# Kernel optimization log

Hardware: AMD Instinct MI355X
Metric: run time of the kernel (lower is better)

## Reference

```python
import jax, jax.numpy as jnp
import numpy as np

KERNEL_MUL = 2.0
KERNEL_NUM = 5


def _mmd(src, tar):
    """Multi-bandwidth Gaussian-kernel MMD, matching torch MMDLoss.mmd."""
    B = src.shape[0]
    total = jnp.concatenate([src, tar], axis=0)          # [2B, D]
    sq = jnp.sum(total * total, axis=1)                  # [2B]
    # ||a-b||^2 = ||a||^2 + ||b||^2 - 2 a.b  (GEMM form of the broadcast subtract)
    dist = sq[:, None] + sq[None, :] - 2.0 * (total @ total.T)  # [2B, 2B]
    n = 2 * B
    # torch uses L2_distance.data -> bandwidth is detached from the graph
    bandwidth = jax.lax.stop_gradient(jnp.sum(dist)) / (n * n - n)
    bandwidth = bandwidth / (KERNEL_MUL ** (KERNEL_NUM // 2))
    kernel = sum(jnp.exp(-dist / (bandwidth * KERNEL_MUL ** k)) for k in range(KERNEL_NUM))
    XX = kernel[:B, :B]
    YY = kernel[B:, B:]
    XY = kernel[:B, B:]
    YX = kernel[B:, :B]
    return jnp.mean(XX + YY - XY - YX)


def setup_inputs() -> dict:
    key = jax.random.key(0)
    k1, k2, k3 = jax.random.split(key, 3)
    B, IN, OUT, L = 4096, 512, 256, 2
    x = jax.random.normal(k1, (B, IN), dtype=jnp.float32)
    W_aux = jax.random.normal(k2, (L, IN), dtype=jnp.float32) * (1.0 / np.sqrt(IN))
    b_aux = jnp.zeros((L,), dtype=jnp.float32)
    W = jax.random.normal(k3, (L, OUT, IN), dtype=jnp.float32) * (1.0 / np.sqrt(IN))
    b = jnp.zeros((L, OUT), dtype=jnp.float32)
    return {"x": x, "W_aux": W_aux, "b_aux": b_aux, "W": W, "b": b}


def reference(x, W_aux, b_aux, W, b):
    L = W.shape[0]
    gates = jax.nn.softmax(x @ W_aux.T + b_aux, axis=-1)      # [B, L]
    outs = jnp.einsum('bi,loi->blo', x, W) + b                # [B, L, out]
    combine = jnp.einsum('bl,blo->bo', gates, outs)           # soft-gated combine
    loss = 0.0
    for i in range(L):
        for j in range(i + 1, L):
            loss = loss + _mmd(outs[:, i, :], outs[:, j, :])
    inter_mmd = loss * 2.0 / (L * L - L)
    return combine, -inter_mmd
```

## Files before the change

kernel.cpp:

```cpp
#include <hip/hip_runtime.h>
#include <stdint.h>
#include <math.h>

typedef __attribute__((ext_vector_type(8))) __bf16 bf16x8;
typedef __attribute__((ext_vector_type(4))) __bf16 bf16x4;
typedef __attribute__((ext_vector_type(4))) float f32x4;

__device__ __forceinline__ void gload_lds16(const __bf16* g, __bf16* l) {
  __builtin_amdgcn_global_load_lds(
      (const __attribute__((address_space(1))) unsigned int*)g,
      (__attribute__((address_space(3))) unsigned int*)l,
      16, 0, 0);
}

__global__ __launch_bounds__(256) void k_gates(const float* __restrict__ x,
                                               const float* __restrict__ Waux,
                                               const float* __restrict__ baux,
                                               float* __restrict__ gates) {
  const int wave = threadIdx.x >> 6;
  const int lane = threadIdx.x & 63;
  const int row = blockIdx.x * 4 + wave;
  const float4* xr = (const float4*)(x + (size_t)row * 512);
  const float4* w0 = (const float4*)(Waux);
  const float4* w1 = (const float4*)(Waux + 512);
  float p0 = 0.f, p1 = 0.f;
  for (int c = lane; c < 128; c += 64) {
    float4 xv = xr[c];
    float4 a = w0[c], b = w1[c];
    p0 += xv.x * a.x + xv.y * a.y + xv.z * a.z + xv.w * a.w;
    p1 += xv.x * b.x + xv.y * b.y + xv.z * b.z + xv.w * b.w;
  }
  for (int off = 32; off; off >>= 1) {
    p0 += __shfl_down(p0, off, 64);
    p1 += __shfl_down(p1, off, 64);
  }
  if (lane == 0) {
    p0 += baux[0]; p1 += baux[1];
    float m = fmaxf(p0, p1);
    float e0 = __expf(p0 - m), e1 = __expf(p1 - m);
    float inv = 1.f / (e0 + e1);
    gates[row * 2 + 0] = e0 * inv;
    gates[row * 2 + 1] = e1 * inv;
  }
}

__global__ __launch_bounds__(256) void k_outs(const float* __restrict__ x,
                                              const float* __restrict__ W,
                                              const float* __restrict__ bias,
                                              __bf16* __restrict__ totalbf) {
  __shared__ __bf16 As[64][64];
  __shared__ __bf16 Bs[64][64];
  const int bj = blockIdx.x;
  const int bi = blockIdx.y;
  const int t = threadIdx.x;
  const int wid = t >> 6, lane = t & 63;
  const int wr = wid >> 1, wc = wid & 1;
  const int n16 = lane & 15, q = lane >> 4;
  const int sx = (n16 & 7) << 3;
  const int erow = t >> 4;
  const int c4 = (t & 15) << 2;

  f32x4 acc[2][2];
  f32x4 zero = {0.f, 0.f, 0.f, 0.f};
  for (int i = 0; i < 2; ++i)
    for (int j = 0; j < 2; ++j) acc[i][j] = zero;

  const int arow0 = bi * 64, brow0 = bj * 64;

  float4 ra[4], rb[4];
#pragma unroll
  for (int p = 0; p < 4; ++p) {
    int row = p * 16 + erow;
    ra[p] = *(const float4*)(x + (size_t)(arow0 + row) * 512 + c4);
    rb[p] = *(const float4*)(W + (size_t)(brow0 + row) * 512 + c4);
  }

  for (int kc = 0; kc < 512; kc += 64) {
#pragma unroll
    for (int p = 0; p < 4; ++p) {
      int row = p * 16 + erow;
      int col = c4 ^ ((row & 7) << 3);
      float4 va = ra[p];
      bf16x4 ba = {(__bf16)va.x, (__bf16)va.y, (__bf16)va.z, (__bf16)va.w};
      *(bf16x4*)&As[row][col] = ba;
      float4 vb = rb[p];
      bf16x4 bb = {(__bf16)vb.x, (__bf16)vb.y, (__bf16)vb.z, (__bf16)vb.w};
      *(bf16x4*)&Bs[row][col] = bb;
    }
    if (kc < 448) {
#pragma unroll
      for (int p = 0; p < 4; ++p) {
        int row = p * 16 + erow;
        ra[p] = *(const float4*)(x + (size_t)(arow0 + row) * 512 + kc + 64 + c4);
        rb[p] = *(const float4*)(W + (size_t)(brow0 + row) * 512 + kc + 64 + c4);
      }
    }
    __syncthreads();
#pragma unroll
    for (int ks = 0; ks < 2; ++ks) {
      bf16x8 af[2], bfr[2];
#pragma unroll
      for (int f = 0; f < 2; ++f) {
        af[f]  = *(const bf16x8*)&As[wr * 32 + f * 16 + n16][(ks * 32 + q * 8) ^ sx];
        bfr[f] = *(const bf16x8*)&Bs[wc * 32 + f * 16 + n16][(ks * 32 + q * 8) ^ sx];
      }
      for (int fr = 0; fr < 2; ++fr)
        for (int fc = 0; fc < 2; ++fc)
          acc[fr][fc] = __builtin_amdgcn_mfma_f32_16x16x32_bf16(af[fr], bfr[fc], acc[fr][fc], 0, 0, 0);
    }
    __syncthreads();
  }

  for (int fc = 0; fc < 2; ++fc) {
    int n_g = bj * 64 + wc * 32 + fc * 16 + n16;
    float bv = bias[n_g];
    int l = n_g >> 8, o = n_g & 255;
    for (int fr = 0; fr < 2; ++fr) {
      for (int r = 0; r < 4; ++r) {
        int m_g = bi * 64 + wr * 32 + fr * 16 + q * 4 + r;
        float v = acc[fr][fc][r] + bv;
        totalbf[(size_t)(l * 4096 + m_g) * 256 + o] = (__bf16)v;
      }
    }
  }
}

__global__ __launch_bounds__(256) void k_sqc(const __bf16* __restrict__ tot,
                                             const float* __restrict__ gates,
                                             float* __restrict__ sq,
                                             float* __restrict__ colsum,
                                             float* __restrict__ out) {
  __shared__ float lcol[4][256];
  const int t = threadIdx.x;
  const int wave = t >> 6, lane = t & 63;
  float c0 = 0.f, c1 = 0.f, c2 = 0.f, c3 = 0.f;
  for (int it = 0; it < 8; ++it) {
    int m = blockIdx.x * 32 + wave * 8 + it;
    bf16x4 v0 = *(const bf16x4*)(tot + (size_t)m * 256 + lane * 4);
    bf16x4 v1 = *(const bf16x4*)(tot + (size_t)(4096 + m) * 256 + lane * 4);
    float f00 = v0[0], f01 = v0[1], f02 = v0[2], f03 = v0[3];
    float f10 = v1[0], f11 = v1[1], f12 = v1[2], f13 = v1[3];
    float s0 = f00 * f00 + f01 * f01 + f02 * f02 + f03 * f03;
    float s1 = f10 * f10 + f11 * f11 + f12 * f12 + f13 * f13;
    for (int off = 32; off; off >>= 1) {
      s0 += __shfl_down(s0, off, 64);
      s1 += __shfl_down(s1, off, 64);
    }
    if (lane == 0) { sq[m] = s0; sq[4096 + m] = s1; }
    c0 += f00 + f10; c1 += f01 + f11; c2 += f02 + f12; c3 += f03 + f13;
    float2 gv = *(const float2*)(gates + m * 2);
    float4 r;
    r.x = gv.x * f00 + gv.y * f10;
    r.y = gv.x * f01 + gv.y * f11;
    r.z = gv.x * f02 + gv.y * f12;
    r.w = gv.x * f03 + gv.y * f13;
    *(float4*)(out + (size_t)m * 256 + lane * 4) = r;
  }
  lcol[wave][lane * 4 + 0] = c0;
  lcol[wave][lane * 4 + 1] = c1;
  lcol[wave][lane * 4 + 2] = c2;
  lcol[wave][lane * 4 + 3] = c3;
  __syncthreads();
  float s2 = lcol[0][t] + lcol[1][t] + lcol[2][t] + lcol[3][t];
  atomicAdd(&colsum[t], s2);
}

__global__ __launch_bounds__(256) void k_bw(const float* __restrict__ sq,
                                            const float* __restrict__ colsum,
                                            float* __restrict__ scal) {
  __shared__ float red[256];
  const int t = threadIdx.x;
  float s = 0.f;
  for (int i = t; i < 8192; i += 256) s += sq[i];
  red[t] = s;
  __syncthreads();
  for (int off = 128; off; off >>= 1) { if (t < off) red[t] += red[t + off]; __syncthreads(); }
  float sumsq = red[0];
  __syncthreads();
  float c = colsum[t];
  red[t] = c * c;
  __syncthreads();
  for (int off = 128; off; off >>= 1) { if (t < off) red[t] += red[t + off]; __syncthreads(); }
  if (t == 0) {
    double sumdist = 2.0 * 8192.0 * (double)sumsq - 2.0 * (double)red[0];
    double bw = sumdist / (8192.0 * 8192.0 - 8192.0) / 4.0;
    scal[1] = (float)(1.4426950408889634 / (bw * 16.0));
    scal[2] = (float)bw;
  }
}

__global__ __launch_bounds__(256, 4) void k_gram(const __bf16* __restrict__ tot,
                                                 const float* __restrict__ sq,
                                                 const float* __restrict__ scal,
                                                 float* __restrict__ Ssum,
                                                 float* __restrict__ out) {
  const int b = blockIdx.x;
  const int nid = (b & 7) * 260 + (b >> 3);
  int ti = (int)((129.0 - sqrt(129.0 * 129.0 - 8.0 * (double)nid)) * 0.5);
  while (64 * ti - ti * (ti - 1) / 2 > nid) --ti;
  while (64 * (ti + 1) - (ti + 1) * ti / 2 <= nid) ++ti;
  const int tj = ti + (nid - (64 * ti - ti * (ti - 1) / 2));

  __shared__ __bf16 As[128][64];
  __shared__ __bf16 Bs[128][64];
  __shared__ float sqi[128], sqj[128];
  __shared__ float wred[4];
  const int t = threadIdx.x;
  const int wid = t >> 6, lane = t & 63;
  const int wr = wid >> 1, wc = wid & 1;
  const int n16 = lane & 15, q = lane >> 4;
  const int sx = (n16 & 7) << 3;
  const int lr = lane >> 3;
  const int ls = lane & 7;

  const float g = scal[1];
  if (t < 128) sqi[t] = sq[ti * 128 + t] * g;
  else         sqj[t - 128] = sq[tj * 128 + (t - 128)] * g;

  f32x4 acc[4][4];
  f32x4 zero = {0.f, 0.f, 0.f, 0.f};
  for (int i = 0; i < 4; ++i)
    for (int j = 0; j < 4; ++j) acc[i][j] = zero;

  const __bf16* gA = tot + (size_t)(ti * 128 + wid * 32 + lr) * 256 + ((ls ^ lr) << 3);
  const __bf16* gB = tot + (size_t)(tj * 128 + wid * 32 + lr) * 256 + ((ls ^ lr) << 3);

  for (int it = 0; it < 4; ++it) {
    const int kc = it * 64;
#pragma unroll
    for (int p = 0; p < 4; ++p) {
      gload_lds16(gA + p * 8 * 256 + kc, &As[wid * 32 + p * 8][0]);
      gload_lds16(gB + p * 8 * 256 + kc, &Bs[wid * 32 + p * 8][0]);
    }
    __syncthreads();
    __builtin_amdgcn_s_setprio(1);
#pragma unroll
    for (int ks = 0; ks < 2; ++ks) {
      bf16x8 af[4], bfr[4];
#pragma unroll
      for (int f = 0; f < 4; ++f) {
        af[f]  = *(const bf16x8*)&As[wr * 64 + f * 16 + n16][(ks * 32 + q * 8) ^ sx];
        bfr[f] = *(const bf16x8*)&Bs[wc * 64 + f * 16 + n16][(ks * 32 + q * 8) ^ sx];
      }
      for (int fr = 0; fr < 4; ++fr)
        for (int fc = 0; fc < 4; ++fc)
          acc[fr][fc] = __builtin_amdgcn_mfma_f32_16x16x32_bf16(af[fr], bfr[fc], acc[fr][fc], 0, 0, 0);
    }
    __builtin_amdgcn_s_setprio(0);
    __syncthreads();
  }

  const float twog = 2.f * g;
  float lsum = 0.f;
  for (int fr = 0; fr < 4; ++fr) {
    for (int r = 0; r < 4; ++r) {
      float gsi = sqi[wr * 64 + fr * 16 + q * 4 + r];
      for (int fc = 0; fc < 4; ++fc) {
        float gsj = sqj[wc * 64 + fc * 16 + n16];
        float u = exp2f(fmaf(twog, acc[fr][fc][r], -(gsi + gsj)));
        float u2 = u * u, u4 = u2 * u2, u8 = u4 * u4;
        float s1 = fmaf(u8, u8, u8);
        lsum += (u + u2) + (u4 + s1);
      }
    }
  }
  for (int off = 32; off; off >>= 1) lsum += __shfl_down(lsum, off, 64);
  if (lane == 0) wred[wid] = lsum;
  __syncthreads();
  if (t == 0) {
    float blocksum = wred[0] + wred[1] + wred[2] + wred[3];
    float sgn = ((ti < 32) == (tj < 32)) ? 1.f : -1.f;
    float wgt = (ti == tj) ? sgn : 2.f * sgn;
    atomicAdd(Ssum, wgt * blocksum);
    __threadfence();
    unsigned int* cnt = (unsigned int*)(Ssum + 3);
    unsigned int c = atomicAdd(cnt, 1u);
    if (c == 2079u) {
      float totS = atomicAdd(Ssum, 0.0f);
      out[1048576] = -(totS / 16777216.0f);
    }
  }
}

extern "C" void kernel_launch(void* const* d_in, const int* in_sizes, int n_in,
                              void* d_out, int out_size, void* d_ws, size_t ws_size,
                              hipStream_t stream) {
  const float* x    = (const float*)d_in[0];
  const float* Waux = (const float*)d_in[1];
  const float* baux = (const float*)d_in[2];
  const float* W    = (const float*)d_in[3];
  const float* bias = (const float*)d_in[4];
  float* out = (float*)d_out;

  char* ws = (char*)d_ws;
  __bf16* totalbf = (__bf16*)ws;
  float* sq      = (float*)(ws + 4194304);
  float* colsum  = (float*)(ws + 4227072);
  float* scal    = (float*)(ws + 4228096);
  float* gates   = (float*)(ws + 4228160);

  hipMemsetAsync(ws + 4227072, 0, 1024 + 64, stream);

  k_gates<<<1024, 256, 0, stream>>>(x, Waux, baux, gates);
  k_outs<<<dim3(8, 64), 256, 0, stream>>>(x, W, bias, totalbf);
  k_sqc<<<128, 256, 0, stream>>>(totalbf, gates, sq, colsum, out);
  k_bw<<<1, 256, 0, stream>>>(sq, colsum, scal);
  k_gram<<<2080, 256, 0, stream>>>(totalbf, sq, scal, scal, out);
}
```

Before: 172.9 us.

## Double-buffer gram tiles, fold bandwidth reduction into sqc, drop memset launch

```diff
diff --git a/kernel.cpp b/kernel.cpp
--- a/kernel.cpp
+++ b/kernel.cpp
@@ -16,7 +16,13 @@
 __global__ __launch_bounds__(256) void k_gates(const float* __restrict__ x,
                                                const float* __restrict__ Waux,
                                                const float* __restrict__ baux,
-                                               float* __restrict__ gates) {
+                                               float* __restrict__ gates,
+                                               float* __restrict__ colsum,
+                                               float* __restrict__ scal) {
+  if (blockIdx.x == 0) {
+    colsum[threadIdx.x] = 0.f;
+    if (threadIdx.x < 8) scal[threadIdx.x] = 0.f;
+  }
   const int wave = threadIdx.x >> 6;
   const int lane = threadIdx.x & 63;
   const int row = blockIdx.x * 4 + wave;
@@ -87,6 +93,7 @@
       bf16x4 bb = {(__bf16)vb.x, (__bf16)vb.y, (__bf16)vb.z, (__bf16)vb.w};
       *(bf16x4*)&Bs[row][col] = bb;
     }
+    __syncthreads();
     if (kc < 448) {
 #pragma unroll
       for (int p = 0; p < 4; ++p) {
@@ -95,7 +102,6 @@
         rb[p] = *(const float4*)(W + (size_t)(brow0 + row) * 512 + kc + 64 + c4);
       }
     }
-    __syncthreads();
 #pragma unroll
     for (int ks = 0; ks < 2; ++ks) {
       bf16x8 af[2], bfr[2];
@@ -129,11 +135,15 @@
                                              const float* __restrict__ gates,
                                              float* __restrict__ sq,
                                              float* __restrict__ colsum,
+                                             float* __restrict__ scal,
                                              float* __restrict__ out) {
   __shared__ float lcol[4][256];
+  __shared__ float wsq[4];
+  __shared__ unsigned int isLast;
   const int t = threadIdx.x;
   const int wave = t >> 6, lane = t & 63;
   float c0 = 0.f, c1 = 0.f, c2 = 0.f, c3 = 0.f;
+  float bsq = 0.f;
   for (int it = 0; it < 8; ++it) {
     int m = blockIdx.x * 32 + wave * 8 + it;
     bf16x4 v0 = *(const bf16x4*)(tot + (size_t)m * 256 + lane * 4);
@@ -146,7 +156,7 @@
       s0 += __shfl_down(s0, off, 64);
       s1 += __shfl_down(s1, off, 64);
     }
-    if (lane == 0) { sq[m] = s0; sq[4096 + m] = s1; }
+    if (lane == 0) { sq[m] = s0; sq[4096 + m] = s1; bsq += s0 + s1; }
     c0 += f00 + f10; c1 += f01 + f11; c2 += f02 + f12; c3 += f03 + f13;
     float2 gv = *(const float2*)(gates + m * 2);
     float4 r;
@@ -160,40 +170,41 @@
   lcol[wave][lane * 4 + 1] = c1;
   lcol[wave][lane * 4 + 2] = c2;
   lcol[wave][lane * 4 + 3] = c3;
+  if (lane == 0) wsq[wave] = bsq;
   __syncthreads();
   float s2 = lcol[0][t] + lcol[1][t] + lcol[2][t] + lcol[3][t];
   atomicAdd(&colsum[t], s2);
-}
-
-__global__ __launch_bounds__(256) void k_bw(const float* __restrict__ sq,
-                                            const float* __restrict__ colsum,
-                                            float* __restrict__ scal) {
-  __shared__ float red[256];
-  const int t = threadIdx.x;
-  float s = 0.f;
-  for (int i = t; i < 8192; i += 256) s += sq[i];
-  red[t] = s;
+  if (t == 0) atomicAdd(&scal[4], wsq[0] + wsq[1] + wsq[2] + wsq[3]);
+  __threadfence();
+  if (t == 0) {
+    unsigned int c = atomicAdd((unsigned int*)(scal + 5), 1u);
+    isLast = (c == 127u) ? 1u : 0u;
+  }
   __syncthreads();
-  for (int off = 128; off; off >>= 1) { if (t < off) red[t] += red[t + off]; __syncthreads(); }
-  float sumsq = red[0];
-  __syncthreads();
-  float c = colsum[t];
-  red[t] = c * c;
-  __syncthreads();
-  for (int off = 128; off; off >>= 1) { if (t < off) red[t] += red[t + off]; __syncthreads(); }
-  if (t == 0) {
-    double sumdist = 2.0 * 8192.0 * (double)sumsq - 2.0 * (double)red[0];
-    double bw = sumdist / (8192.0 * 8192.0 - 8192.0) / 4.0;
-    scal[1] = (float)(1.4426950408889634 / (bw * 16.0));
-    scal[2] = (float)bw;
-  }
-}
-
-__global__ __launch_bounds__(256, 4) void k_gram(const __bf16* __restrict__ tot,
-                                                 const float* __restrict__ sq,
-                                                 const float* __restrict__ scal,
-                                                 float* __restrict__ Ssum,
-                                                 float* __restrict__ out) {
+  if (isLast) {
+    __threadfence();
+    float cv = atomicAdd(&colsum[t], 0.0f);
+    lcol[0][t] = cv * cv;
+    __syncthreads();
+    for (int off = 128; off; off >>= 1) {
+      if (t < off) lcol[0][t] += lcol[0][t + off];
+      __syncthreads();
+    }
+    if (t == 0) {
+      float sumsq = atomicAdd(&scal[4], 0.0f);
+      double sumdist = 2.0 * 8192.0 * (double)sumsq - 2.0 * (double)lcol[0][0];
+      double bw = sumdist / (8192.0 * 8192.0 - 8192.0) / 4.0;
+      scal[1] = (float)(1.4426950408889634 / (bw * 16.0));
+      scal[2] = (float)bw;
+    }
+  }
+}
+
+__global__ __launch_bounds__(256) void k_gram(const __bf16* __restrict__ tot,
+                                              const float* __restrict__ sq,
+                                              const float* __restrict__ scal,
+                                              float* __restrict__ Ssum,
+                                              float* __restrict__ out) {
   const int b = blockIdx.x;
   const int nid = (b & 7) * 260 + (b >> 3);
   int ti = (int)((129.0 - sqrt(129.0 * 129.0 - 8.0 * (double)nid)) * 0.5);
@@ -201,8 +212,8 @@
   while (64 * (ti + 1) - (ti + 1) * ti / 2 <= nid) ++ti;
   const int tj = ti + (nid - (64 * ti - ti * (ti - 1) / 2));
 
-  __shared__ __bf16 As[128][64];
-  __shared__ __bf16 Bs[128][64];
+  __shared__ __bf16 As[2][128][64];
+  __shared__ __bf16 Bs[2][128][64];
   __shared__ float sqi[128], sqj[128];
   __shared__ float wred[4];
   const int t = threadIdx.x;
@@ -225,29 +236,44 @@
   const __bf16* gA = tot + (size_t)(ti * 128 + wid * 32 + lr) * 256 + ((ls ^ lr) << 3);
   const __bf16* gB = tot + (size_t)(tj * 128 + wid * 32 + lr) * 256 + ((ls ^ lr) << 3);
 
+#pragma unroll
+  for (int p = 0; p < 4; ++p) {
+    gload_lds16(gA + p * 8 * 256, &As[0][wid * 32 + p * 8][0]);
+    gload_lds16(gB + p * 8 * 256, &Bs[0][wid * 32 + p * 8][0]);
+  }
+
+#pragma unroll
   for (int it = 0; it < 4; ++it) {
-    const int kc = it * 64;
-#pragma unroll
-    for (int p = 0; p < 4; ++p) {
-      gload_lds16(gA + p * 8 * 256 + kc, &As[wid * 32 + p * 8][0]);
-      gload_lds16(gB + p * 8 * 256 + kc, &Bs[wid * 32 + p * 8][0]);
-    }
-    __syncthreads();
+    const int cur = it & 1;
+    if (it < 3) {
+      const int kc = (it + 1) * 64;
+#pragma unroll
+      for (int p = 0; p < 4; ++p) {
+        gload_lds16(gA + p * 8 * 256 + kc, &As[cur ^ 1][wid * 32 + p * 8][0]);
+        gload_lds16(gB + p * 8 * 256 + kc, &Bs[cur ^ 1][wid * 32 + p * 8][0]);
+      }
+    }
+    if (it < 3) asm volatile("s_waitcnt vmcnt(8)" ::: "memory");
+    else        asm volatile("s_waitcnt vmcnt(0)" ::: "memory");
+    __builtin_amdgcn_s_barrier();
+    __builtin_amdgcn_sched_barrier(0);
     __builtin_amdgcn_s_setprio(1);
 #pragma unroll
     for (int ks = 0; ks < 2; ++ks) {
       bf16x8 af[4], bfr[4];
 #pragma unroll
       for (int f = 0; f < 4; ++f) {
-        af[f]  = *(const bf16x8*)&As[wr * 64 + f * 16 + n16][(ks * 32 + q * 8) ^ sx];
-        bfr[f] = *(const bf16x8*)&Bs[wc * 64 + f * 16 + n16][(ks * 32 + q * 8) ^ sx];
+        af[f]  = *(const bf16x8*)&As[cur][wr * 64 + f * 16 + n16][(ks * 32 + q * 8) ^ sx];
+        bfr[f] = *(const bf16x8*)&Bs[cur][wc * 64 + f * 16 + n16][(ks * 32 + q * 8) ^ sx];
       }
       for (int fr = 0; fr < 4; ++fr)
         for (int fc = 0; fc < 4; ++fc)
           acc[fr][fc] = __builtin_amdgcn_mfma_f32_16x16x32_bf16(af[fr], bfr[fc], acc[fr][fc], 0, 0, 0);
     }
     __builtin_amdgcn_s_setprio(0);
-    __syncthreads();
+    asm volatile("s_waitcnt lgkmcnt(0)" ::: "memory");
+    __builtin_amdgcn_sched_barrier(0);
+    __builtin_amdgcn_s_barrier();
   }
 
   const float twog = 2.f * g;
@@ -299,11 +325,8 @@
   float* scal    = (float*)(ws + 4228096);
   float* gates   = (float*)(ws + 4228160);
 
-  hipMemsetAsync(ws + 4227072, 0, 1024 + 64, stream);
-
-  k_gates<<<1024, 256, 0, stream>>>(x, Waux, baux, gates);
+  k_gates<<<1024, 256, 0, stream>>>(x, Waux, baux, gates, colsum, scal);
   k_outs<<<dim3(8, 64), 256, 0, stream>>>(x, W, bias, totalbf);
-  k_sqc<<<128, 256, 0, stream>>>(totalbf, gates, sq, colsum, out);
-  k_bw<<<1, 256, 0, stream>>>(sq, colsum, scal);
+  k_sqc<<<128, 256, 0, stream>>>(totalbf, gates, sq, colsum, scal, out);
   k_gram<<<2080, 256, 0, stream>>>(totalbf, sq, scal, scal, out);
 }
```

After: 173.0 us. About the same (+0.1%).
